# Performance work log

Hardware: AMD Instinct MI355X
Metric: run time of the kernel (lower is better)

The kernel has to match this reference:

```python
import jax, jax.numpy as jnp
import numpy as np

EMBED = 256
HEADS = 8
LEVELS = 4
POINTS = 4
HD = EMBED // HEADS  # 32


def _bilinear_sample(v, grid):
    """torch.F.grid_sample(mode='bilinear', padding_mode='zeros', align_corners=False).
    v: (B, C, H, W); grid: (B, Q, P, 2) with xy coords in [-1, 1].
    Returns (B, C, Q, P).
    """
    B, C, H, W = v.shape
    x = (grid[..., 0] + 1.0) * (W * 0.5) - 0.5
    y = (grid[..., 1] + 1.0) * (H * 0.5) - 0.5
    x0f = jnp.floor(x)
    y0f = jnp.floor(y)
    wx = x - x0f
    wy = y - y0f
    x0 = x0f.astype(jnp.int32)
    y0 = y0f.astype(jnp.int32)
    vf = v.reshape(B, C, H * W)

    def corner(xi, yi, w):
        valid = (xi >= 0) & (xi < W) & (yi >= 0) & (yi < H)
        idx = jnp.clip(yi, 0, H - 1) * W + jnp.clip(xi, 0, W - 1)  # (B, Q, P)
        g = jax.vmap(lambda vb, ib: jnp.take(vb, ib, axis=1))(vf, idx.reshape(B, -1))
        g = g.reshape(B, C, idx.shape[1], idx.shape[2])  # (B, C, Q, P)
        return g * (w * valid.astype(v.dtype))[:, None]

    return (corner(x0, y0, (1 - wx) * (1 - wy))
            + corner(x0 + 1, y0, wx * (1 - wy))
            + corner(x0, y0 + 1, (1 - wx) * wy)
            + corner(x0 + 1, y0 + 1, wx * wy))


def setup_inputs() -> dict:
    key = jax.random.key(0)
    ks = jax.random.split(key, 16)
    N, Q, D = 2, 8192, EMBED
    inp = {
        'query': jax.random.normal(ks[0], (N, Q, D), jnp.float32),
        'feat0': jax.random.normal(ks[1], (N, D, 64, 64), jnp.float32),
        'feat1': jax.random.normal(ks[2], (N, D, 32, 32), jnp.float32),
        'feat2': jax.random.normal(ks[3], (N, D, 16, 16), jnp.float32),
        'feat3': jax.random.normal(ks[4], (N, D, 8, 8), jnp.float32),
        'reference_points': jax.random.uniform(ks[5], (N, Q, 2), jnp.float32),
        # params stored as (in, out); equivalent math to torch Linear's x @ W.T + b
        'W_off': jax.random.normal(ks[6], (D, HEADS * LEVELS * POINTS * 2), jnp.float32) * 0.01,
        'b_off': jax.random.normal(ks[7], (HEADS * LEVELS * POINTS * 2,), jnp.float32) * 0.01,
        'W_attn': jax.random.normal(ks[8], (D, HEADS * LEVELS * POINTS), jnp.float32) * 0.02,
        'b_attn': jax.random.normal(ks[9], (HEADS * LEVELS * POINTS,), jnp.float32) * 0.02,
        'W_val': jax.random.normal(ks[10], (D, D), jnp.float32) * (1.0 / np.sqrt(D)),
        'b_val': jnp.zeros((D,), jnp.float32),
        'W_out': jax.random.normal(ks[11], (D, D), jnp.float32) * (1.0 / np.sqrt(D)),
        'b_out': jnp.zeros((D,), jnp.float32),
    }
    return inp


def reference(query, feat0, feat1, feat2, feat3, reference_points,
              W_off, b_off, W_attn, b_attn, W_val, b_val, W_out, b_out):
    feats = [feat0, feat1, feat2, feat3]
    N, Q, D = query.shape
    # offset / attention-weight projections
    off = (query @ W_off + b_off).reshape(N, Q, HEADS, LEVELS, POINTS, 2)
    attn = (query @ W_attn + b_attn).reshape(N, Q, HEADS, LEVELS, POINTS)
    # reference points (N,Q,2) -> (N,Q,L,2)
    ref = jnp.broadcast_to(reference_points[:, :, None, :], (N, Q, LEVELS, 2))
    # value projection (1x1 conv) per level, split heads -> (N*H, hd, H_l, W_l)
    vals = [(jnp.einsum('bchw,cd->bdhw', f, W_val) + b_val[None, :, None, None])
            .reshape(N * HEADS, HD, f.shape[2], f.shape[3]) for f in feats]
    # flatten batch*heads
    off = off.transpose(0, 2, 1, 3, 4, 5).reshape(N * HEADS, Q, LEVELS, POINTS, 2)
    attn = attn.transpose(0, 2, 1, 3, 4).reshape(N * HEADS, Q, LEVELS, POINTS)
    refh = jnp.broadcast_to(ref[:, None], (N, HEADS, Q, LEVELS, 2)).reshape(N * HEADS, Q, LEVELS, 2)
    loc = refh[:, :, :, None, :] + off                 # (NH, Q, L, P, 2) in [0,1]
    grid = 2.0 * loc - 1.0                             # [-1, 1]
    # per-level bilinear sampling -> (NH, hd, Q, L, P)
    sampled = jnp.stack([_bilinear_sample(vals[l], grid[:, :, l]) for l in range(LEVELS)], axis=-2)
    # softmax over levels*points
    aw = jax.nn.softmax(attn.reshape(N * HEADS, Q, LEVELS * POINTS), axis=-1)
    aw = jnp.nan_to_num(aw).reshape(N * HEADS, Q, LEVELS, POINTS)
    out = jnp.einsum('bcqlp,bqlp->bcq', sampled, aw)   # (NH, hd, Q)
    out = out.reshape(N, HEADS, HD, Q).transpose(0, 3, 1, 2).reshape(N, Q, D)
    return out @ W_out + b_out
```

## Files before the change

kernel.cpp:

```cpp
#include <hip/hip_runtime.h>
#include <math.h>

#define NB 2
#define QN 8192
#define DIM 256
#define S_TOT 5440

typedef unsigned int uint32;
typedef _Float16 f16;
typedef __attribute__((ext_vector_type(8))) _Float16 h8;
typedef __attribute__((ext_vector_type(2))) _Float16 h2;
typedef __attribute__((ext_vector_type(4))) float f32x4;

__device__ __forceinline__ h2 shfl_h2(h2 v, int mask) {
  union { h2 h; int i; } u; u.h = v;
  u.i = __shfl_xor(u.i, mask);
  return u.h;
}
__device__ __forceinline__ int pack_h2(float w) {
  union { h2 h; int i; } u; const f16 wh = (f16)w; u.h = h2{wh, wh};
  return u.i;
}


__global__ __launch_bounds__(256) void prep_kernel(
    const float* __restrict__ q,
    const float* __restrict__ f0, const float* __restrict__ f1,
    const float* __restrict__ f2, const float* __restrict__ f3,
    const float* __restrict__ W_off, const float* __restrict__ W_attn,
    const float* __restrict__ W_val, const float* __restrict__ W_out,
    f16* __restrict__ qf, f16* __restrict__ featT_f,
    f16* __restrict__ Wcat_f, f16* __restrict__ Wval_f, f16* __restrict__ Wout_f) {
  const int t = blockIdx.x, y = blockIdx.y, tid = threadIdx.x;

  if (t < 128) {
    const int row0 = (t * 8 + y) * 16;
    const int s_l = tid >> 4, c8 = tid & 15;
    const float* src = q + (size_t)(row0 + s_l) * 256;
#pragma unroll
    for (int cc = 0; cc < 2; ++cc) {
      const int c8c = c8 + cc * 16;
      const float4 u0 = *(const float4*)(src + c8c * 8);
      const float4 u1 = *(const float4*)(src + c8c * 8 + 4);
      h8 hv = {(f16)u0.x, (f16)u0.y, (f16)u0.z, (f16)u0.w,
               (f16)u1.x, (f16)u1.y, (f16)u1.z, (f16)u1.w};
      *(h8*)(qf + ((size_t)(row0 >> 4) * 32 + c8c) * 128 + s_l * 8) = hv;
    }
    return;
  }

  __shared__ float tile[32][33];
  const int tx = tid & 31, ty = tid >> 5;
  const float* src;
  f16* dst;
  int S, tb, s_base = 0;

  if (t < 468) {
    const int tt0 = t - 128;
    const int b = (tt0 >= 170) ? 1 : 0;
    const int tt = tt0 - 170 * b;
    int soff;
    if (tt < 128)      { src = f0; S = 4096; soff = 0;    tb = tt; }
    else if (tt < 160) { src = f1; S = 1024; soff = 4096; tb = tt - 128; }
    else if (tt < 168) { src = f2; S = 256;  soff = 5120; tb = tt - 160; }
    else               { src = f3; S = 64;   soff = 5376; tb = tt - 168; }
    src += (size_t)b * 256 * S;
    dst = featT_f;
    s_base = b * S_TOT + soff;
  } else {
    const int tw = t - 468;
    if (tw < 8)       { src = W_off;  dst = Wcat_f; S = 256; tb = tw;      s_base = 0; }
    else if (tw < 12) { src = W_attn; dst = Wcat_f; S = 128; tb = tw - 8;  s_base = 256; }
    else if (tw < 20) { src = W_val;  dst = Wval_f; S = 256; tb = tw - 12; s_base = 0; }
    else              { src = W_out;  dst = Wout_f; S = 256; tb = tw - 20; s_base = 0; }
  }
  const int s0 = tb * 32, c0 = y * 32;

#pragma unroll
  for (int j = 0; j < 4; ++j) {
    const int c = c0 + ty + j * 8;
    tile[ty + j * 8][tx] = src[(size_t)c * S + s0 + tx];
  }
  __syncthreads();

  if (tid < 128) {
    const int s_l = tid >> 2, c8l = tid & 3;
    const int Sg = s_base + s0 + s_l;
    const int c8 = (c0 >> 3) + c8l;
    h8 v;
#pragma unroll
    for (int j = 0; j < 8; ++j) v[j] = (f16)tile[c8l * 8 + j][s_l];
    *(h8*)(dst + ((size_t)(Sg >> 4) * 32 + c8) * 128 + (Sg & 15) * 8) = v;
  }
}

__global__ __launch_bounds__(256) void gemm_fused_kernel(
    const f16* __restrict__ qf, const f16* __restrict__ featT_f,
    const f16* __restrict__ Wcat_f, const f16* __restrict__ Wval_f,
    const float* __restrict__ b_val, const float* __restrict__ b_off,
    const float* __restrict__ b_attn,
    f16* __restrict__ vals, f16* __restrict__ offb, f16* __restrict__ attnb) {
  const int t = blockIdx.x;
  const int tid = threadIdx.x;
  const int lane = tid & 63, wid = tid >> 6;
  const int l15 = lane & 15, l4 = lane >> 4;

  if (t < 340) {
    const int g0 = t * 2;
    f32x4 acc[2][4] = {};
#pragma unroll
    for (int ks = 0; ks < 8; ++ks) {
      const int s2 = ks * 4 + l4;
      h8 a[2], b[4];
#pragma unroll
      for (int m = 0; m < 2; ++m)
        a[m] = *(const h8*)(featT_f + ((size_t)(g0 + m) * 32 + s2) * 128 + l15 * 8);
#pragma unroll
      for (int n = 0; n < 4; ++n)
        b[n] = *(const h8*)(Wval_f + ((size_t)(wid * 4 + n) * 32 + s2) * 128 + l15 * 8);
#pragma unroll
      for (int m = 0; m < 2; ++m)
#pragma unroll
        for (int n = 0; n < 4; ++n)
          acc[m][n] = __builtin_amdgcn_mfma_f32_16x16x32_f16(a[m], b[n], acc[m][n], 0, 0, 0);
    }
#pragma unroll
    for (int m = 0; m < 2; ++m)
#pragma unroll
      for (int n = 0; n < 4; ++n)
#pragma unroll
        for (int r = 0; r < 4; ++r) {
          const size_t rw = (size_t)t * 32 + m * 16 + l4 * 4 + r;
          const int col = wid * 64 + n * 16 + l15;
          vals[rw * 256 + col] = (f16)(acc[m][n][r] + b_val[col]);
        }
  } else {
    const int t2 = t - 340;
    const int g0 = t2 * 2;
    f32x4 acc[2][6] = {};
#pragma unroll
    for (int ks = 0; ks < 8; ++ks) {
      const int s2 = ks * 4 + l4;
      h8 a[2], b[6];
#pragma unroll
      for (int m = 0; m < 2; ++m)
        a[m] = *(const h8*)(qf + ((size_t)(g0 + m) * 32 + s2) * 128 + l15 * 8);
#pragma unroll
      for (int n = 0; n < 6; ++n)
        b[n] = *(const h8*)(Wcat_f + ((size_t)(wid * 6 + n) * 32 + s2) * 128 + l15 * 8);
#pragma unroll
      for (int m = 0; m < 2; ++m)
#pragma unroll
        for (int n = 0; n < 6; ++n)
          acc[m][n] = __builtin_amdgcn_mfma_f32_16x16x32_f16(a[m], b[n], acc[m][n], 0, 0, 0);
    }
#pragma unroll
    for (int m = 0; m < 2; ++m)
#pragma unroll
      for (int n = 0; n < 6; ++n)
#pragma unroll
        for (int r = 0; r < 4; ++r) {
          const size_t rw = (size_t)t2 * 32 + m * 16 + l4 * 4 + r;
          const int col = wid * 96 + n * 16 + l15;
          const float v = acc[m][n][r];
          if (col < 256)
            offb[rw * 256 + col] = (f16)(v + b_off[col]);
          else
            attnb[rw * 128 + (col - 256)] = (f16)(v + b_attn[col - 256]);
        }
  }
}

__global__ __launch_bounds__(256) void gemm_out_kernel(
    const f16* __restrict__ A, const f16* __restrict__ Bt,
    const float* __restrict__ bias, float* __restrict__ out) {
  const int tid = threadIdx.x;
  const int lane = tid & 63, wid = tid >> 6;
  const int l15 = lane & 15, l4 = lane >> 4;
  const int g0 = blockIdx.x * 2;

  f32x4 acc[2][4] = {};
#pragma unroll
  for (int ks = 0; ks < 8; ++ks) {
    const int s2 = ks * 4 + l4;
    h8 a[2], b[4];
#pragma unroll
    for (int m = 0; m < 2; ++m)
      a[m] = *(const h8*)(A + ((size_t)(g0 + m) * 32 + s2) * 128 + l15 * 8);
#pragma unroll
    for (int n = 0; n < 4; ++n)
      b[n] = *(const h8*)(Bt + ((size_t)(wid * 4 + n) * 32 + s2) * 128 + l15 * 8);
#pragma unroll
    for (int m = 0; m < 2; ++m)
#pragma unroll
      for (int n = 0; n < 4; ++n)
        acc[m][n] = __builtin_amdgcn_mfma_f32_16x16x32_f16(a[m], b[n], acc[m][n], 0, 0, 0);
  }

#pragma unroll
  for (int m = 0; m < 2; ++m)
#pragma unroll
    for (int n = 0; n < 4; ++n)
#pragma unroll
      for (int r = 0; r < 4; ++r) {
        const size_t rw = (size_t)blockIdx.x * 32 + m * 16 + l4 * 4 + r;
        const int col = wid * 64 + n * 16 + l15;
        out[rw * 256 + col] = acc[m][n][r] + bias[col];
      }
}

__global__ __launch_bounds__(256) void sample_kernel(
    const f16* __restrict__ vals, const f16* __restrict__ offb,
    const f16* __restrict__ attnb, const float* __restrict__ refp,
    f16* __restrict__ samp_f) {
  const int tid = threadIdx.x;
  const int g = tid & 15;
  const int grp = tid >> 4;
  const int h = grp & 7;
  const int half = tid >> 7;
  const int bq = blockIdx.x * 2 + half;
  const int b = bq >> 13;

  __shared__ int4 wts2[16][17];
  __shared__ int4 idxs[16][17];

  const float rx = refp[(size_t)bq * 2 + 0];
  const float ry = refp[(size_t)bq * 2 + 1];

  float logit = (float)attnb[(size_t)bq * 128 + h * 16 + g];
  float m = logit;
#pragma unroll
  for (int mask = 1; mask < 16; mask <<= 1)
    m = fmaxf(m, __shfl_xor(m, mask, 16));
  const float e = __expf(logit - m);
  float ssum = e;
#pragma unroll
  for (int mask = 1; mask < 16; mask <<= 1)
    ssum += __shfl_xor(ssum, mask, 16);
  const float aw = e / ssum;

  const h2 ov = *(const h2*)(offb + (size_t)bq * 256 + h * 32 + g * 2);
  const int l = g >> 2;
  const int Wl = 64 >> l;
  const int loff = (l == 0) ? 0 : (l == 1) ? 4096 : (l == 2) ? 5120 : 5376;

  const float px = (rx + (float)ov[0]) * (float)Wl - 0.5f;
  const float py = (ry + (float)ov[1]) * (float)Wl - 0.5f;
  const float fx = floorf(px), fy = floorf(py);
  const float wx = px - fx, wy = py - fy;
  const int x0 = (int)fx, y0 = (int)fy;
  const int x1 = x0 + 1, y1 = y0 + 1;
  const float vx0 = (x0 >= 0 && x0 < Wl) ? 1.f : 0.f;
  const float vx1 = (x1 >= 0 && x1 < Wl) ? 1.f : 0.f;
  const float vy0 = (y0 >= 0 && y0 < Wl) ? 1.f : 0.f;
  const float vy1 = (y1 >= 0 && y1 < Wl) ? 1.f : 0.f;
  const int cx0 = min(max(x0, 0), Wl - 1), cx1 = min(max(x1, 0), Wl - 1);
  const int cy0 = min(max(y0, 0), Wl - 1), cy1 = min(max(y1, 0), Wl - 1);
  const int base = b * S_TOT + loff;
  idxs[grp][g] = make_int4((base + cy0 * Wl + cx0) * 512,
                           (base + cy0 * Wl + cx1) * 512,
                           (base + cy1 * Wl + cx0) * 512,
                           (base + cy1 * Wl + cx1) * 512);
  wts2[grp][g] = make_int4(pack_h2(aw * (1.f - wx) * (1.f - wy) * vx0 * vy0),
                           pack_h2(aw * wx * (1.f - wy) * vx1 * vy0),
                           pack_h2(aw * (1.f - wx) * wy * vx0 * vy1),
                           pack_h2(aw * wx * wy * vx1 * vy1));
  __syncthreads();

  const int c4 = g & 3, pc = g >> 2;
  const char* vb = (const char*)vals + (h * 64 + c4 * 16);

  int wv[16];
  int ids[16];
#pragma unroll
  for (int pt = 0; pt < 16; ++pt) {
    wv[pt] = ((const int*)&wts2[grp][pt])[pc];
    ids[pt] = ((const int*)&idxs[grp][pt])[pc];
  }
  h8 vv[16];
#pragma unroll
  for (int pt = 0; pt < 16; ++pt) vv[pt] = *(const h8*)(vb + ids[pt]);

  h2 a2[4] = {};
#pragma unroll
  for (int pt = 0; pt < 16; ++pt) {
    union { int i; h2 h; } w; w.i = wv[pt];
    const h2* vp = (const h2*)&vv[pt];
    a2[0] += vp[0] * w.h;
    a2[1] += vp[1] * w.h;
    a2[2] += vp[2] * w.h;
    a2[3] += vp[3] * w.h;
  }
#pragma unroll
  for (int j = 0; j < 4; ++j) {
    a2[j] += shfl_h2(a2[j], 4);
    a2[j] += shfl_h2(a2[j], 8);
  }
  if (pc == 0) {
    h8 r = {a2[0][0], a2[0][1], a2[1][0], a2[1][1],
            a2[2][0], a2[2][1], a2[3][0], a2[3][1]};
    *(h8*)(samp_f + ((size_t)(bq >> 4) * 32 + h * 4 + c4) * 128 + (bq & 15) * 8) = r;
  }
}

extern "C" void kernel_launch(void* const* d_in, const int* in_sizes, int n_in,
                              void* d_out, int out_size, void* d_ws, size_t ws_size,
                              hipStream_t stream) {
  const float* query = (const float*)d_in[0];
  const float* feat[4] = {(const float*)d_in[1], (const float*)d_in[2],
                          (const float*)d_in[3], (const float*)d_in[4]};
  const float* refp  = (const float*)d_in[5];
  const float* W_off = (const float*)d_in[6];
  const float* b_off = (const float*)d_in[7];
  const float* W_attn = (const float*)d_in[8];
  const float* b_attn = (const float*)d_in[9];
  const float* W_val = (const float*)d_in[10];
  const float* b_val = (const float*)d_in[11];
  const float* W_out = (const float*)d_in[12];
  const float* b_out = (const float*)d_in[13];
  float* out = (float*)d_out;

  f16* ws = (f16*)d_ws;
  f16* vals    = ws;
  f16* offb    = vals + (size_t)NB * S_TOT * 256;
  f16* attnb   = offb + (size_t)NB * QN * 256;
  f16* qf      = attnb + (size_t)NB * QN * 128;
  f16* samp_f  = qf;
  f16* featT_f = qf + (size_t)NB * QN * 256;
  f16* Wcat_f  = featT_f + (size_t)NB * S_TOT * 256;
  f16* Wval_f  = Wcat_f + 384 * 256;
  f16* Wout_f  = Wval_f + 256 * 256;

  prep_kernel<<<dim3(496, 8), 256, 0, stream>>>(
      query, feat[0], feat[1], feat[2], feat[3],
      W_off, W_attn, W_val, W_out, qf, featT_f, Wcat_f, Wval_f, Wout_f);

  gemm_fused_kernel<<<340 + 512, 256, 0, stream>>>(
      qf, featT_f, Wcat_f, Wval_f, b_val, b_off, b_attn, vals, offb, attnb);

  sample_kernel<<<(NB * QN) / 2, 256, 0, stream>>>(vals, offb, attnb, refp, samp_f);

  gemm_out_kernel<<<(NB * QN) / 32, 256, 0, stream>>>(samp_f, Wout_f, b_out, out);
}
```

Measured before the change: 68.20 us.

## Bucket-sort queries by reference point and restructure sampler thread mapping

Queries are counting-sorted into 16x16 spatial buckets by reference point, using a histogram built in the GEMM kernel and a new scan-and-scatter kernel. The sampler then processes 8 queries per block in sorted order so that nearby gathers share L2/L1 lines. The sampler thread mapping also changes: each thread handles 4 points and all 16 points for its channel slice, which removes the cross-lane reduction shuffles. In exchange this adds an extra kernel launch, atomics, and non-deterministic perm order within buckets, and it reads the perm indirection.

```diff
diff --git a/kernel.cpp b/kernel.cpp
--- a/kernel.cpp
+++ b/kernel.cpp
@@ -9,17 +9,19 @@
 typedef unsigned int uint32;
 typedef _Float16 f16;
 typedef __attribute__((ext_vector_type(8))) _Float16 h8;
+typedef __attribute__((ext_vector_type(4))) _Float16 h4;
 typedef __attribute__((ext_vector_type(2))) _Float16 h2;
 typedef __attribute__((ext_vector_type(4))) float f32x4;
 
-__device__ __forceinline__ h2 shfl_h2(h2 v, int mask) {
-  union { h2 h; int i; } u; u.h = v;
-  u.i = __shfl_xor(u.i, mask);
-  return u.h;
-}
 __device__ __forceinline__ int pack_h2(float w) {
   union { h2 h; int i; } u; const f16 wh = (f16)w; u.h = h2{wh, wh};
   return u.i;
+}
+__device__ __forceinline__ int bucket_of(const float* refp, int q) {
+  const float rx = refp[(size_t)q * 2], ry = refp[(size_t)q * 2 + 1];
+  const int bx = min(15, max(0, (int)(rx * 16.f)));
+  const int by = min(15, max(0, (int)(ry * 16.f)));
+  return ((q >> 13) << 8) | (by << 4) | bx;
 }
 
 
@@ -30,8 +32,15 @@
     const float* __restrict__ W_off, const float* __restrict__ W_attn,
     const float* __restrict__ W_val, const float* __restrict__ W_out,
     f16* __restrict__ qf, f16* __restrict__ featT_f,
-    f16* __restrict__ Wcat_f, f16* __restrict__ Wval_f, f16* __restrict__ Wout_f) {
+    f16* __restrict__ Wcat_f, f16* __restrict__ Wval_f, f16* __restrict__ Wout_f,
+    int* __restrict__ hist, int* __restrict__ cnt) {
   const int t = blockIdx.x, y = blockIdx.y, tid = threadIdx.x;
+
+  if (t == 496) {
+    hist[tid] = 0; hist[tid + 256] = 0;
+    cnt[tid] = 0;  cnt[tid + 256] = 0;
+    return;
+  }
 
   if (t < 128) {
     const int row0 = (t * 8 + y) * 16;
@@ -98,12 +107,19 @@
     const f16* __restrict__ qf, const f16* __restrict__ featT_f,
     const f16* __restrict__ Wcat_f, const f16* __restrict__ Wval_f,
     const float* __restrict__ b_val, const float* __restrict__ b_off,
-    const float* __restrict__ b_attn,
-    f16* __restrict__ vals, f16* __restrict__ offb, f16* __restrict__ attnb) {
+    const float* __restrict__ b_attn, const float* __restrict__ refp,
+    f16* __restrict__ vals, f16* __restrict__ offb, f16* __restrict__ attnb,
+    int* __restrict__ hist) {
   const int t = blockIdx.x;
   const int tid = threadIdx.x;
   const int lane = tid & 63, wid = tid >> 6;
   const int l15 = lane & 15, l4 = lane >> 4;
+
+  if (t >= 852) {
+    const int q = (t - 852) * 256 + tid;
+    atomicAdd(&hist[bucket_of(refp, q)], 1);
+    return;
+  }
 
   if (t < 340) {
     const int g0 = t * 2;
@@ -171,6 +187,29 @@
   }
 }
 
+__global__ __launch_bounds__(256) void sort_kernel(
+    const float* __restrict__ refp, const int* __restrict__ hist,
+    int* __restrict__ cnt, int* __restrict__ perm) {
+  __shared__ int sc[512];
+  const int tid = threadIdx.x;
+  sc[tid] = hist[tid];
+  sc[tid + 256] = hist[tid + 256];
+  __syncthreads();
+  for (int off = 1; off < 512; off <<= 1) {
+    const int t0 = (tid >= off) ? sc[tid - off] : 0;
+    const int t1 = (tid + 256 >= off) ? sc[tid + 256 - off] : 0;
+    __syncthreads();
+    sc[tid] += t0;
+    sc[tid + 256] += t1;
+    __syncthreads();
+  }
+  const int q = blockIdx.x * 256 + tid;
+  const int bk = bucket_of(refp, q);
+  const int base = bk ? sc[bk - 1] : 0;
+  const int r = atomicAdd(&cnt[bk], 1);
+  perm[base + r] = q;
+}
+
 __global__ __launch_bounds__(256) void gemm_out_kernel(
     const f16* __restrict__ A, const f16* __restrict__ Bt,
     const float* __restrict__ bias, float* __restrict__ out) {
@@ -212,95 +251,104 @@
 __global__ __launch_bounds__(256) void sample_kernel(
     const f16* __restrict__ vals, const f16* __restrict__ offb,
     const f16* __restrict__ attnb, const float* __restrict__ refp,
-    f16* __restrict__ samp_f) {
+    const int* __restrict__ perm, f16* __restrict__ samp_f) {
   const int tid = threadIdx.x;
-  const int g = tid & 15;
-  const int grp = tid >> 4;
-  const int h = grp & 7;
-  const int half = tid >> 7;
-  const int bq = blockIdx.x * 2 + half;
+  const int qi = tid >> 5, hh = (tid >> 2) & 7, c4 = tid & 3;
+
+  __shared__ int4 wts2[8][8][16];
+  __shared__ int4 idxs[8][8][16];
+  __shared__ int qbq[8];
+
+  if (tid < 8) qbq[tid] = perm[blockIdx.x * 8 + tid];
+  __syncthreads();
+
+  const int bq = qbq[qi];
   const int b = bq >> 13;
 
-  __shared__ int4 wts2[16][17];
-  __shared__ int4 idxs[16][17];
-
-  const float rx = refp[(size_t)bq * 2 + 0];
-  const float ry = refp[(size_t)bq * 2 + 1];
-
-  float logit = (float)attnb[(size_t)bq * 128 + h * 16 + g];
-  float m = logit;
-#pragma unroll
-  for (int mask = 1; mask < 16; mask <<= 1)
-    m = fmaxf(m, __shfl_xor(m, mask, 16));
-  const float e = __expf(logit - m);
-  float ssum = e;
-#pragma unroll
-  for (int mask = 1; mask < 16; mask <<= 1)
-    ssum += __shfl_xor(ssum, mask, 16);
-  const float aw = e / ssum;
-
-  const h2 ov = *(const h2*)(offb + (size_t)bq * 256 + h * 32 + g * 2);
-  const int l = g >> 2;
-  const int Wl = 64 >> l;
-  const int loff = (l == 0) ? 0 : (l == 1) ? 4096 : (l == 2) ? 5120 : 5376;
-
-  const float px = (rx + (float)ov[0]) * (float)Wl - 0.5f;
-  const float py = (ry + (float)ov[1]) * (float)Wl - 0.5f;
-  const float fx = floorf(px), fy = floorf(py);
-  const float wx = px - fx, wy = py - fy;
-  const int x0 = (int)fx, y0 = (int)fy;
-  const int x1 = x0 + 1, y1 = y0 + 1;
-  const float vx0 = (x0 >= 0 && x0 < Wl) ? 1.f : 0.f;
-  const float vx1 = (x1 >= 0 && x1 < Wl) ? 1.f : 0.f;
-  const float vy0 = (y0 >= 0 && y0 < Wl) ? 1.f : 0.f;
-  const float vy1 = (y1 >= 0 && y1 < Wl) ? 1.f : 0.f;
-  const int cx0 = min(max(x0, 0), Wl - 1), cx1 = min(max(x1, 0), Wl - 1);
-  const int cy0 = min(max(y0, 0), Wl - 1), cy1 = min(max(y1, 0), Wl - 1);
-  const int base = b * S_TOT + loff;
-  idxs[grp][g] = make_int4((base + cy0 * Wl + cx0) * 512,
-                           (base + cy0 * Wl + cx1) * 512,
-                           (base + cy1 * Wl + cx0) * 512,
-                           (base + cy1 * Wl + cx1) * 512);
-  wts2[grp][g] = make_int4(pack_h2(aw * (1.f - wx) * (1.f - wy) * vx0 * vy0),
-                           pack_h2(aw * wx * (1.f - wy) * vx1 * vy0),
-                           pack_h2(aw * (1.f - wx) * wy * vx0 * vy1),
-                           pack_h2(aw * wx * wy * vx1 * vy1));
+  {
+    const float rx = refp[(size_t)bq * 2 + 0];
+    const float ry = refp[(size_t)bq * 2 + 1];
+    const int pt0 = c4 * 4;
+
+    const h4 lg = *(const h4*)(attnb + (size_t)bq * 128 + hh * 16 + pt0);
+    float logit[4], e[4];
+    float m = -1e30f;
+#pragma unroll
+    for (int p = 0; p < 4; ++p) { logit[p] = (float)lg[p]; m = fmaxf(m, logit[p]); }
+    m = fmaxf(m, __shfl_xor(m, 1));
+    m = fmaxf(m, __shfl_xor(m, 2));
+    float s = 0.f;
+#pragma unroll
+    for (int p = 0; p < 4; ++p) { e[p] = __expf(logit[p] - m); s += e[p]; }
+    s += __shfl_xor(s, 1);
+    s += __shfl_xor(s, 2);
+    const float inv = 1.0f / s;
+
+    const h8 ov = *(const h8*)(offb + (size_t)bq * 256 + hh * 32 + pt0 * 2);
+    const int l = c4;
+    const int Wl = 64 >> l;
+    const int loff = (l == 0) ? 0 : (l == 1) ? 4096 : (l == 2) ? 5120 : 5376;
+    const int base = b * S_TOT + loff;
+
+#pragma unroll
+    for (int p = 0; p < 4; ++p) {
+      const float aw = e[p] * inv;
+      const float px = (rx + (float)ov[p * 2 + 0]) * (float)Wl - 0.5f;
+      const float py = (ry + (float)ov[p * 2 + 1]) * (float)Wl - 0.5f;
+      const float fx = floorf(px), fy = floorf(py);
+      const float wx = px - fx, wy = py - fy;
+      const int x0 = (int)fx, y0 = (int)fy;
+      const int x1 = x0 + 1, y1 = y0 + 1;
+      const float vx0 = (x0 >= 0 && x0 < Wl) ? 1.f : 0.f;
+      const float vx1 = (x1 >= 0 && x1 < Wl) ? 1.f : 0.f;
+      const float vy0 = (y0 >= 0 && y0 < Wl) ? 1.f : 0.f;
+      const float vy1 = (y1 >= 0 && y1 < Wl) ? 1.f : 0.f;
+      const int cx0 = min(max(x0, 0), Wl - 1), cx1 = min(max(x1, 0), Wl - 1);
+      const int cy0 = min(max(y0, 0), Wl - 1), cy1 = min(max(y1, 0), Wl - 1);
+      idxs[qi][hh][pt0 + p] = make_int4((base + cy0 * Wl + cx0) * 512,
+                                        (base + cy0 * Wl + cx1) * 512,
+                                        (base + cy1 * Wl + cx0) * 512,
+                                        (base + cy1 * Wl + cx1) * 512);
+      wts2[qi][hh][pt0 + p] = make_int4(pack_h2(aw * (1.f - wx) * (1.f - wy) * vx0 * vy0),
+                                        pack_h2(aw * wx * (1.f - wy) * vx1 * vy0),
+                                        pack_h2(aw * (1.f - wx) * wy * vx0 * vy1),
+                                        pack_h2(aw * wx * wy * vx1 * vy1));
+    }
+  }
   __syncthreads();
 
-  const int c4 = g & 3, pc = g >> 2;
-  const char* vb = (const char*)vals + (h * 64 + c4 * 16);
-
-  int wv[16];
-  int ids[16];
-#pragma unroll
-  for (int pt = 0; pt < 16; ++pt) {
-    wv[pt] = ((const int*)&wts2[grp][pt])[pc];
-    ids[pt] = ((const int*)&idxs[grp][pt])[pc];
-  }
-  h8 vv[16];
-#pragma unroll
-  for (int pt = 0; pt < 16; ++pt) vv[pt] = *(const h8*)(vb + ids[pt]);
-
+  const char* vb = (const char*)vals + (hh * 64 + c4 * 16);
   h2 a2[4] = {};
-#pragma unroll
-  for (int pt = 0; pt < 16; ++pt) {
-    union { int i; h2 h; } w; w.i = wv[pt];
-    const h2* vp = (const h2*)&vv[pt];
-    a2[0] += vp[0] * w.h;
-    a2[1] += vp[1] * w.h;
-    a2[2] += vp[2] * w.h;
-    a2[3] += vp[3] * w.h;
-  }
-#pragma unroll
-  for (int j = 0; j < 4; ++j) {
-    a2[j] += shfl_h2(a2[j], 4);
-    a2[j] += shfl_h2(a2[j], 8);
-  }
-  if (pc == 0) {
-    h8 r = {a2[0][0], a2[0][1], a2[1][0], a2[1][1],
-            a2[2][0], a2[2][1], a2[3][0], a2[3][1]};
-    *(h8*)(samp_f + ((size_t)(bq >> 4) * 32 + h * 4 + c4) * 128 + (bq & 15) * 8) = r;
-  }
+
+#pragma unroll
+  for (int ch = 0; ch < 4; ++ch) {
+    int ids[16], wv[16];
+#pragma unroll
+    for (int p = 0; p < 4; ++p) {
+      const int4 iv = idxs[qi][hh][ch * 4 + p];
+      const int4 wv4 = wts2[qi][hh][ch * 4 + p];
+      ids[p * 4 + 0] = iv.x; ids[p * 4 + 1] = iv.y;
+      ids[p * 4 + 2] = iv.z; ids[p * 4 + 3] = iv.w;
+      wv[p * 4 + 0] = wv4.x; wv[p * 4 + 1] = wv4.y;
+      wv[p * 4 + 2] = wv4.z; wv[p * 4 + 3] = wv4.w;
+    }
+    h8 vv[16];
+#pragma unroll
+    for (int j = 0; j < 16; ++j) vv[j] = *(const h8*)(vb + ids[j]);
+#pragma unroll
+    for (int j = 0; j < 16; ++j) {
+      union { int i; h2 h; } w; w.i = wv[j];
+      const h2* vp = (const h2*)&vv[j];
+      a2[0] += vp[0] * w.h;
+      a2[1] += vp[1] * w.h;
+      a2[2] += vp[2] * w.h;
+      a2[3] += vp[3] * w.h;
+    }
+  }
+
+  h8 r = {a2[0][0], a2[0][1], a2[1][0], a2[1][1],
+          a2[2][0], a2[2][1], a2[3][0], a2[3][1]};
+  *(h8*)(samp_f + ((size_t)(bq >> 4) * 32 + hh * 4 + c4) * 128 + (bq & 15) * 8) = r;
 }
 
 extern "C" void kernel_launch(void* const* d_in, const int* in_sizes, int n_in,
@@ -330,15 +378,23 @@
   f16* Wcat_f  = featT_f + (size_t)NB * S_TOT * 256;
   f16* Wval_f  = Wcat_f + 384 * 256;
   f16* Wout_f  = Wval_f + 256 * 256;
-
-  prep_kernel<<<dim3(496, 8), 256, 0, stream>>>(
+  int* hist    = (int*)(Wout_f + 256 * 256);
+  int* cnt     = hist + 512;
+  int* perm    = cnt + 512;
+
+  prep_kernel<<<dim3(497, 8), 256, 0, stream>>>(
       query, feat[0], feat[1], feat[2], feat[3],
-      W_off, W_attn, W_val, W_out, qf, featT_f, Wcat_f, Wval_f, Wout_f);
-
-  gemm_fused_kernel<<<340 + 512, 256, 0, stream>>>(
-      qf, featT_f, Wcat_f, Wval_f, b_val, b_off, b_attn, vals, offb, attnb);
-
-  sample_kernel<<<(NB * QN) / 2, 256, 0, stream>>>(vals, offb, attnb, refp, samp_f);
+      W_off, W_attn, W_val, W_out, qf, featT_f, Wcat_f, Wval_f, Wout_f,
+      hist, cnt);
+
+  gemm_fused_kernel<<<852 + 64, 256, 0, stream>>>(
+      qf, featT_f, Wcat_f, Wval_f, b_val, b_off, b_attn, refp,
+      vals, offb, attnb, hist);
+
+  sort_kernel<<<64, 256, 0, stream>>>(refp, hist, cnt, perm);
+
+  sample_kernel<<<(NB * QN) / 8, 256, 0, stream>>>(
+      vals, offb, attnb, refp, perm, samp_f);
 
   gemm_out_kernel<<<(NB * QN) / 32, 256, 0, stream>>>(samp_f, Wout_f, b_out, out);
 }
```

Result: slower. 76.93 us (+12.8%).

## Fuse bilinear sampling with output projection GEMM via shared-memory tile

Applied to the files above, without the earlier changes.

Merges the sampling kernel and the output projection GEMM into one kernel. Each block samples 32 queries in 16 sequential chunks into an LDS tile, then multiplies it by W_out with MFMA. This removes the global round-trip of the sampled intermediate and one launch, but cuts the grid from thousands of blocks to 512 and serializes the gathers per block, reducing latency hiding.

```diff
diff --git a/kernel.cpp b/kernel.cpp
--- a/kernel.cpp
+++ b/kernel.cpp
@@ -171,136 +171,141 @@
   }
 }
 
-__global__ __launch_bounds__(256) void gemm_out_kernel(
-    const f16* __restrict__ A, const f16* __restrict__ Bt,
-    const float* __restrict__ bias, float* __restrict__ out) {
-  const int tid = threadIdx.x;
-  const int lane = tid & 63, wid = tid >> 6;
-  const int l15 = lane & 15, l4 = lane >> 4;
-  const int g0 = blockIdx.x * 2;
-
-  f32x4 acc[2][4] = {};
-#pragma unroll
-  for (int ks = 0; ks < 8; ++ks) {
-    const int s2 = ks * 4 + l4;
-    h8 a[2], b[4];
-#pragma unroll
-    for (int m = 0; m < 2; ++m)
-      a[m] = *(const h8*)(A + ((size_t)(g0 + m) * 32 + s2) * 128 + l15 * 8);
-#pragma unroll
-    for (int n = 0; n < 4; ++n)
-      b[n] = *(const h8*)(Bt + ((size_t)(wid * 4 + n) * 32 + s2) * 128 + l15 * 8);
-#pragma unroll
-    for (int m = 0; m < 2; ++m)
-#pragma unroll
-      for (int n = 0; n < 4; ++n)
-        acc[m][n] = __builtin_amdgcn_mfma_f32_16x16x32_f16(a[m], b[n], acc[m][n], 0, 0, 0);
-  }
-
-#pragma unroll
-  for (int m = 0; m < 2; ++m)
-#pragma unroll
-    for (int n = 0; n < 4; ++n)
-#pragma unroll
-      for (int r = 0; r < 4; ++r) {
-        const size_t rw = (size_t)blockIdx.x * 32 + m * 16 + l4 * 4 + r;
-        const int col = wid * 64 + n * 16 + l15;
-        out[rw * 256 + col] = acc[m][n][r] + bias[col];
-      }
-}
-
-__global__ __launch_bounds__(256) void sample_kernel(
+__global__ __launch_bounds__(256) void sample_out_kernel(
     const f16* __restrict__ vals, const f16* __restrict__ offb,
     const f16* __restrict__ attnb, const float* __restrict__ refp,
-    f16* __restrict__ samp_f) {
+    const f16* __restrict__ Wout_f, const float* __restrict__ b_out,
+    float* __restrict__ out) {
   const int tid = threadIdx.x;
   const int g = tid & 15;
   const int grp = tid >> 4;
   const int h = grp & 7;
   const int half = tid >> 7;
-  const int bq = blockIdx.x * 2 + half;
-  const int b = bq >> 13;
-
-  __shared__ int4 wts2[16][17];
-  __shared__ int4 idxs[16][17];
-
-  const float rx = refp[(size_t)bq * 2 + 0];
-  const float ry = refp[(size_t)bq * 2 + 1];
-
-  float logit = (float)attnb[(size_t)bq * 128 + h * 16 + g];
-  float m = logit;
-#pragma unroll
-  for (int mask = 1; mask < 16; mask <<= 1)
-    m = fmaxf(m, __shfl_xor(m, mask, 16));
-  const float e = __expf(logit - m);
-  float ssum = e;
-#pragma unroll
-  for (int mask = 1; mask < 16; mask <<= 1)
-    ssum += __shfl_xor(ssum, mask, 16);
-  const float aw = e / ssum;
-
-  const h2 ov = *(const h2*)(offb + (size_t)bq * 256 + h * 32 + g * 2);
-  const int l = g >> 2;
-  const int Wl = 64 >> l;
-  const int loff = (l == 0) ? 0 : (l == 1) ? 4096 : (l == 2) ? 5120 : 5376;
-
-  const float px = (rx + (float)ov[0]) * (float)Wl - 0.5f;
-  const float py = (ry + (float)ov[1]) * (float)Wl - 0.5f;
-  const float fx = floorf(px), fy = floorf(py);
-  const float wx = px - fx, wy = py - fy;
-  const int x0 = (int)fx, y0 = (int)fy;
-  const int x1 = x0 + 1, y1 = y0 + 1;
-  const float vx0 = (x0 >= 0 && x0 < Wl) ? 1.f : 0.f;
-  const float vx1 = (x1 >= 0 && x1 < Wl) ? 1.f : 0.f;
-  const float vy0 = (y0 >= 0 && y0 < Wl) ? 1.f : 0.f;
-  const float vy1 = (y1 >= 0 && y1 < Wl) ? 1.f : 0.f;
-  const int cx0 = min(max(x0, 0), Wl - 1), cx1 = min(max(x1, 0), Wl - 1);
-  const int cy0 = min(max(y0, 0), Wl - 1), cy1 = min(max(y1, 0), Wl - 1);
-  const int base = b * S_TOT + loff;
-  idxs[grp][g] = make_int4((base + cy0 * Wl + cx0) * 512,
-                           (base + cy0 * Wl + cx1) * 512,
-                           (base + cy1 * Wl + cx0) * 512,
-                           (base + cy1 * Wl + cx1) * 512);
-  wts2[grp][g] = make_int4(pack_h2(aw * (1.f - wx) * (1.f - wy) * vx0 * vy0),
-                           pack_h2(aw * wx * (1.f - wy) * vx1 * vy0),
-                           pack_h2(aw * (1.f - wx) * wy * vx0 * vy1),
-                           pack_h2(aw * wx * wy * vx1 * vy1));
-  __syncthreads();
+  const int q0 = blockIdx.x * 32;
+
+  __shared__ int4 wts2[2][16][17];
+  __shared__ int4 idxs[2][16][17];
+  __shared__ f16 samp[64 * 136];
 
   const int c4 = g & 3, pc = g >> 2;
   const char* vb = (const char*)vals + (h * 64 + c4 * 16);
 
-  int wv[16];
-  int ids[16];
-#pragma unroll
-  for (int pt = 0; pt < 16; ++pt) {
-    wv[pt] = ((const int*)&wts2[grp][pt])[pc];
-    ids[pt] = ((const int*)&idxs[grp][pt])[pc];
-  }
-  h8 vv[16];
-#pragma unroll
-  for (int pt = 0; pt < 16; ++pt) vv[pt] = *(const h8*)(vb + ids[pt]);
-
-  h2 a2[4] = {};
-#pragma unroll
-  for (int pt = 0; pt < 16; ++pt) {
-    union { int i; h2 h; } w; w.i = wv[pt];
-    const h2* vp = (const h2*)&vv[pt];
-    a2[0] += vp[0] * w.h;
-    a2[1] += vp[1] * w.h;
-    a2[2] += vp[2] * w.h;
-    a2[3] += vp[3] * w.h;
-  }
-#pragma unroll
-  for (int j = 0; j < 4; ++j) {
-    a2[j] += shfl_h2(a2[j], 4);
-    a2[j] += shfl_h2(a2[j], 8);
-  }
-  if (pc == 0) {
-    h8 r = {a2[0][0], a2[0][1], a2[1][0], a2[1][1],
-            a2[2][0], a2[2][1], a2[3][0], a2[3][1]};
-    *(h8*)(samp_f + ((size_t)(bq >> 4) * 32 + h * 4 + c4) * 128 + (bq & 15) * 8) = r;
-  }
+  for (int chunk = 0; chunk < 16; ++chunk) {
+    const int buf = chunk & 1;
+    const int bq = q0 + chunk * 2 + half;
+    const int b = bq >> 13;
+
+    {
+      const float rx = refp[(size_t)bq * 2 + 0];
+      const float ry = refp[(size_t)bq * 2 + 1];
+
+      float logit = (float)attnb[(size_t)bq * 128 + h * 16 + g];
+      float m = logit;
+#pragma unroll
+      for (int mask = 1; mask < 16; mask <<= 1)
+        m = fmaxf(m, __shfl_xor(m, mask, 16));
+      const float e = __expf(logit - m);
+      float ssum = e;
+#pragma unroll
+      for (int mask = 1; mask < 16; mask <<= 1)
+        ssum += __shfl_xor(ssum, mask, 16);
+      const float aw = e / ssum;
+
+      const h2 ov = *(const h2*)(offb + (size_t)bq * 256 + h * 32 + g * 2);
+      const int l = g >> 2;
+      const int Wl = 64 >> l;
+      const int loff = (l == 0) ? 0 : (l == 1) ? 4096 : (l == 2) ? 5120 : 5376;
+
+      const float px = (rx + (float)ov[0]) * (float)Wl - 0.5f;
+      const float py = (ry + (float)ov[1]) * (float)Wl - 0.5f;
+      const float fx = floorf(px), fy = floorf(py);
+      const float wx = px - fx, wy = py - fy;
+      const int x0 = (int)fx, y0 = (int)fy;
+      const int x1 = x0 + 1, y1 = y0 + 1;
+      const float vx0 = (x0 >= 0 && x0 < Wl) ? 1.f : 0.f;
+      const float vx1 = (x1 >= 0 && x1 < Wl) ? 1.f : 0.f;
+      const float vy0 = (y0 >= 0 && y0 < Wl) ? 1.f : 0.f;
+      const float vy1 = (y1 >= 0 && y1 < Wl) ? 1.f : 0.f;
+      const int cx0 = min(max(x0, 0), Wl - 1), cx1 = min(max(x1, 0), Wl - 1);
+      const int cy0 = min(max(y0, 0), Wl - 1), cy1 = min(max(y1, 0), Wl - 1);
+      const int base = b * S_TOT + loff;
+      idxs[buf][grp][g] = make_int4((base + cy0 * Wl + cx0) * 512,
+                                    (base + cy0 * Wl + cx1) * 512,
+                                    (base + cy1 * Wl + cx0) * 512,
+                                    (base + cy1 * Wl + cx1) * 512);
+      wts2[buf][grp][g] = make_int4(pack_h2(aw * (1.f - wx) * (1.f - wy) * vx0 * vy0),
+                                    pack_h2(aw * wx * (1.f - wy) * vx1 * vy0),
+                                    pack_h2(aw * (1.f - wx) * wy * vx0 * vy1),
+                                    pack_h2(aw * wx * wy * vx1 * vy1));
+    }
+    __syncthreads();
+
+    int wv[16];
+    int ids[16];
+#pragma unroll
+    for (int pt = 0; pt < 16; ++pt) {
+      wv[pt] = ((const int*)&wts2[buf][grp][pt])[pc];
+      ids[pt] = ((const int*)&idxs[buf][grp][pt])[pc];
+    }
+    h8 vv[16];
+#pragma unroll
+    for (int pt = 0; pt < 16; ++pt) vv[pt] = *(const h8*)(vb + ids[pt]);
+
+    h2 a2[4] = {};
+#pragma unroll
+    for (int pt = 0; pt < 16; ++pt) {
+      union { int i; h2 h; } w; w.i = wv[pt];
+      const h2* vp = (const h2*)&vv[pt];
+      a2[0] += vp[0] * w.h;
+      a2[1] += vp[1] * w.h;
+      a2[2] += vp[2] * w.h;
+      a2[3] += vp[3] * w.h;
+    }
+#pragma unroll
+    for (int j = 0; j < 4; ++j) {
+      a2[j] += shfl_h2(a2[j], 4);
+      a2[j] += shfl_h2(a2[j], 8);
+    }
+    if (pc == 0) {
+      h8 r = {a2[0][0], a2[0][1], a2[1][0], a2[1][1],
+              a2[2][0], a2[2][1], a2[3][0], a2[3][1]};
+      const int rl = chunk * 2 + half;
+      *(h8*)&samp[((rl >> 4) * 32 + h * 4 + c4) * 136 + (rl & 15) * 8] = r;
+    }
+  }
+  __syncthreads();
+
+  const int lane = tid & 63, wid = tid >> 6;
+  const int l15 = lane & 15, l4 = lane >> 4;
+
+  f32x4 acc[2][4] = {};
+#pragma unroll
+  for (int ks = 0; ks < 8; ++ks) {
+    const int s2 = ks * 4 + l4;
+    h8 a[2], b[4];
+#pragma unroll
+    for (int m = 0; m < 2; ++m)
+      a[m] = *(const h8*)&samp[(m * 32 + s2) * 136 + l15 * 8];
+#pragma unroll
+    for (int n = 0; n < 4; ++n)
+      b[n] = *(const h8*)(Wout_f + ((size_t)(wid * 4 + n) * 32 + s2) * 128 + l15 * 8);
+#pragma unroll
+    for (int m = 0; m < 2; ++m)
+#pragma unroll
+      for (int n = 0; n < 4; ++n)
+        acc[m][n] = __builtin_amdgcn_mfma_f32_16x16x32_f16(a[m], b[n], acc[m][n], 0, 0, 0);
+  }
+
+#pragma unroll
+  for (int m = 0; m < 2; ++m)
+#pragma unroll
+    for (int n = 0; n < 4; ++n)
+#pragma unroll
+      for (int r = 0; r < 4; ++r) {
+        const size_t rw = (size_t)q0 + m * 16 + l4 * 4 + r;
+        const int col = wid * 64 + n * 16 + l15;
+        out[rw * 256 + col] = acc[m][n][r] + b_out[col];
+      }
 }
 
 extern "C" void kernel_launch(void* const* d_in, const int* in_sizes, int n_in,
@@ -325,7 +330,6 @@
   f16* offb    = vals + (size_t)NB * S_TOT * 256;
   f16* attnb   = offb + (size_t)NB * QN * 256;
   f16* qf      = attnb + (size_t)NB * QN * 128;
-  f16* samp_f  = qf;
   f16* featT_f = qf + (size_t)NB * QN * 256;
   f16* Wcat_f  = featT_f + (size_t)NB * S_TOT * 256;
   f16* Wval_f  = Wcat_f + 384 * 256;
@@ -338,7 +342,6 @@
   gemm_fused_kernel<<<340 + 512, 256, 0, stream>>>(
       qf, featT_f, Wcat_f, Wval_f, b_val, b_off, b_attn, vals, offb, attnb);
 
-  sample_kernel<<<(NB * QN) / 2, 256, 0, stream>>>(vals, offb, attnb, refp, samp_f);
-
-  gemm_out_kernel<<<(NB * QN) / 32, 256, 0, stream>>>(samp_f, Wout_f, b_out, out);
-}
+  sample_out_kernel<<<(NB * QN) / 32, 256, 0, stream>>>(
+      vals, offb, attnb, refp, Wout_f, b_out, out);
+}
```

Result: slower. 73.99 us (+8.5%).
